# Kernel tuning notes

Measured on AMD Instinct MI355X. Metric: run time of the kernel, lower is better.

The kernel has to match this reference:

```python
import jax, jax.numpy as jnp
import numpy as np

N, E = 50000, 500000
HID, H, D = 128, 8, 16
ED, EGD = 32, 64


def _ln(x, g, b):
    m = x.mean(-1, keepdims=True)
    v = ((x - m) ** 2).mean(-1, keepdims=True)
    return (x - m) / jnp.sqrt(v + 1e-5) * g + b


def _gelu(x):
    return jax.nn.gelu(x, approximate=False)  # torch nn.GELU default (erf)


def setup_inputs() -> dict:
    key = jax.random.key(0)
    ks = jax.random.split(key, 24)
    s = lambda k, shape, scale=0.05: jax.random.normal(k, shape, jnp.float32) * scale
    inp = {
        "x": jax.random.normal(ks[0], (N, HID), jnp.float32),
        "edge_attr": jax.random.normal(ks[1], (E, ED), jnp.float32),
        "gamma": jax.random.uniform(ks[2], (N, HID), jnp.float32),
        "beta": jax.random.normal(ks[3], (N, HID), jnp.float32) * 0.1,
        "Wq": s(ks[4], (HID, H * D)),
        "Wk": s(ks[5], (HID, H * D)),
        "Wv": s(ks[6], (HID, H * D)),
        "Wo": s(ks[7], (H * D, HID)),
        "bo": jnp.zeros((HID,), jnp.float32),
        "ea_w1": s(ks[8], (ED, EGD)), "ea_b1": jnp.zeros((EGD,), jnp.float32),
        "ea_w2": s(ks[9], (EGD, H)), "ea_b2": jnp.zeros((H,), jnp.float32),
        "eg_w1": s(ks[10], (ED, EGD)), "eg_b1": jnp.zeros((EGD,), jnp.float32),
        "eg_w2": s(ks[11], (EGD, H * D)), "eg_b2": jnp.zeros((H * D,), jnp.float32),
        "ln1_g": jnp.ones((HID,), jnp.float32), "ln1_b": jnp.zeros((HID,), jnp.float32),
        "ln2_g": jnp.ones((HID,), jnp.float32), "ln2_b": jnp.zeros((HID,), jnp.float32),
        "ffn_w1": s(ks[12], (HID, 2 * HID)), "ffn_b1": jnp.zeros((2 * HID,), jnp.float32),
        "ffn_w2": s(ks[13], (2 * HID, HID)), "ffn_b2": jnp.zeros((HID,), jnp.float32),
        "edge_index": jax.random.randint(ks[14], (2, E), 0, N, jnp.int32),
    }
    return inp


def reference(x, edge_attr, gamma, beta, Wq, Wk, Wv, Wo, bo,
              ea_w1, ea_b1, ea_w2, ea_b2, eg_w1, eg_b1, eg_w2, eg_b2,
              ln1_g, ln1_b, ln2_g, ln2_b, ffn_w1, ffn_b1, ffn_w2, ffn_b2,
              edge_index):
    n = x.shape[0]
    src, dst = edge_index[0], edge_index[1]
    xn = _ln(x, ln1_g, ln1_b)
    Q = (xn @ Wq).reshape(n, H, D)
    K = (xn @ Wk).reshape(n, H, D)
    V = (xn @ Wv).reshape(n, H, D)
    # per-edge attention logits [E, H]
    logits = (Q[dst] * K[src]).sum(-1) * (D ** -0.5)
    logits = logits + (_gelu(edge_attr @ ea_w1 + ea_b1) @ ea_w2 + ea_b2)
    # sparse softmax over edges sharing a destination; torch version
    # initializes max buffer to zeros (include_self), so clamp max at 0
    m = jnp.maximum(jax.ops.segment_max(logits, dst, num_segments=n), 0.0)
    ex = jnp.exp(logits - m[dst])
    ssum = jax.ops.segment_sum(ex, dst, num_segments=n)
    attn = ex / (ssum[dst] + 1e-10)
    gate = jax.nn.sigmoid(_gelu(edge_attr @ eg_w1 + eg_b1) @ eg_w2 + eg_b2).reshape(-1, H, D)
    weighted = attn[..., None] * (gate * V[src])  # [E, H, D]
    agg = jax.ops.segment_sum(weighted, dst, num_segments=n).reshape(n, H * D)
    out = agg @ Wo + bo
    out = gamma * out + beta
    x = x + out
    x2 = _ln(x, ln2_g, ln2_b)
    f = _gelu(x2 @ ffn_w1 + ffn_b1) @ ffn_w2 + ffn_b2
    return x + f
```

## Files before the change

kernel.cpp:

```cpp
#include <hip/hip_runtime.h>

constexpr int N   = 50000;
constexpr int E   = 500000;
constexpr int HID = 128;
constexpr int NH  = 8;
constexpr int ED  = 32;
constexpr int EGD = 64;
constexpr int NB  = (N + 255) / 256;

typedef short  bf16x8 __attribute__((ext_vector_type(8)));
typedef float  f32x4  __attribute__((ext_vector_type(4)));

__device__ __forceinline__ float gelu_f(float v) {
    float u = v * v;
    float a = v * fmaf(u, -0.07135481283f, -1.5957691216f);
    float e = __expf(a);
    return v * __builtin_amdgcn_rcpf(1.f + e);
}
__device__ __forceinline__ float sigm_f(float v) {
    float e = __expf(-v);
    return __builtin_amdgcn_rcpf(1.f + e);
}
__device__ __forceinline__ unsigned short f2bf(float f) {
    unsigned int u = __float_as_uint(f);
    return (unsigned short)((u + 0x7fffu + ((u >> 16) & 1u)) >> 16);
}
__device__ __forceinline__ unsigned int cvt_pk_bf16(float lo, float hi) {
    unsigned int r;
    asm("v_cvt_pk_bf16_f32 %0, %1, %2" : "=v"(r) : "v"(lo), "v"(hi));
    return r;
}
__device__ __forceinline__ float dot2(unsigned int a, unsigned int b) {
    float al = __uint_as_float(a << 16), ah = __uint_as_float(a & 0xffff0000u);
    float bl = __uint_as_float(b << 16), bh = __uint_as_float(b & 0xffff0000u);
    return al * bl + ah * bh;
}

__global__ __launch_bounds__(256) void k_cvt(
    const float* __restrict__ Wq, const float* __restrict__ Wk,
    const float* __restrict__ Wv, const float* __restrict__ Wo,
    const float* __restrict__ fw1, const float* __restrict__ fw2,
    const float* __restrict__ ea_w1, const float* __restrict__ ea_w2,
    const float* __restrict__ eg_w1, const float* __restrict__ eg_w2,
    unsigned short* __restrict__ dst)
{
    int f = blockIdx.x * 256 + threadIdx.x;
    if (f >= 18048) return;
    const float* W; int KT, srcN, base;
    if      (f < 2048)  { W = Wq;    KT = 4; srcN = 128; base = 0; }
    else if (f < 4096)  { W = Wk;    KT = 4; srcN = 128; base = 2048; }
    else if (f < 6144)  { W = Wv;    KT = 4; srcN = 128; base = 4096; }
    else if (f < 8192)  { W = Wo;    KT = 4; srcN = 128; base = 6144; }
    else if (f < 12288) { W = fw1;   KT = 4; srcN = 256; base = 8192; }
    else if (f < 16384) { W = fw2;   KT = 8; srcN = 128; base = 12288; }
    else if (f < 16640) { W = ea_w1; KT = 1; srcN = 64;  base = 16384; }
    else if (f < 16768) { W = ea_w2; KT = 2; srcN = 8;   base = 16640; }
    else if (f < 17024) { W = eg_w1; KT = 1; srcN = 64;  base = 16768; }
    else                { W = eg_w2; KT = 2; srcN = 128; base = 17024; }
    int fl = f - base, lane = fl & 63, t = fl >> 6;
    int ks = t % KT, nt = t / KT;
    int n  = nt * 16 + (lane & 15);
    int k0 = ks * 32 + (lane >> 4) * 8;
    union { unsigned short u[8]; uint4 v; } o;
#pragma unroll
    for (int j = 0; j < 8; j++)
        o.u[j] = (n < srcN) ? f2bf(W[(size_t)(k0 + j) * srcN + n]) : (unsigned short)0;
    *(uint4*)(dst + (size_t)f * 8) = o.v;
}

__global__ __launch_bounds__(256) void k_ln_qkv_mfma(
    const float* __restrict__ x, const float* __restrict__ g1, const float* __restrict__ b1,
    const unsigned short* __restrict__ wqkv,
    unsigned short* __restrict__ Q, unsigned short* __restrict__ K, unsigned short* __restrict__ V)
{
    __shared__ unsigned short xn_lds[64 * 128];
    const int tid = threadIdx.x;
    const int nodeBase = blockIdx.x * 64;

    {
        int nl = tid >> 2, q = tid & 3;
        int gn = nodeBase + nl; if (gn >= N) gn = N - 1;
        const float4* xp = (const float4*)(x + (size_t)gn * HID + q * 32);
        float xv[32]; float s = 0.f, ss = 0.f;
#pragma unroll
        for (int i = 0; i < 8; i++) {
            float4 t = xp[i];
            xv[4*i] = t.x; xv[4*i+1] = t.y; xv[4*i+2] = t.z; xv[4*i+3] = t.w;
        }
#pragma unroll
        for (int i = 0; i < 32; i++) { s += xv[i]; ss += xv[i] * xv[i]; }
        s += __shfl_xor(s, 1); ss += __shfl_xor(ss, 1);
        s += __shfl_xor(s, 2); ss += __shfl_xor(ss, 2);
        float mean = s * (1.f / HID);
        float ri = rsqrtf(ss * (1.f / HID) - mean * mean + 1e-5f);
#pragma unroll
        for (int j = 0; j < 4; j++) {
            union { unsigned short u[8]; uint4 v4; } o;
#pragma unroll
            for (int c = 0; c < 8; c++) {
                int col = q * 32 + j * 8 + c;
                o.u[c] = f2bf((xv[j*8+c] - mean) * ri * g1[col] + b1[col]);
            }
            int phys = (q * 4 + j) ^ (nl & 15);
            *(uint4*)&xn_lds[nl * 128 + phys * 8] = o.v4;
        }
    }
    __syncthreads();

    const int lane = tid & 63, w = tid >> 6, lm = lane & 15, kb = lane >> 4;
    bf16x8 af[4];
#pragma unroll
    for (int ks = 0; ks < 4; ks++)
        af[ks] = *(const bf16x8*)&xn_lds[(w * 16 + lm) * 128 + ((ks * 4 + kb) ^ lm) * 8];

    for (int nt = 0; nt < 24; nt++) {
        f32x4 c = {0.f, 0.f, 0.f, 0.f};
#pragma unroll
        for (int ks = 0; ks < 4; ks++)
            c = __builtin_amdgcn_mfma_f32_16x16x32_bf16(
                    af[ks], *(const bf16x8*)&wqkv[((size_t)(nt * 4 + ks) * 64 + lane) * 8],
                    c, 0, 0, 0);
        unsigned short* O = (nt < 8) ? Q : ((nt < 16) ? K : V);
        int cc = (nt & 7) * 16 + lm;
#pragma unroll
        for (int r = 0; r < 4; r++) {
            int node = nodeBase + w * 16 + kb * 4 + r;
            if (node < N) O[(size_t)node * HID + cc] = f2bf(c[r]);
        }
    }
}

__global__ __launch_bounds__(256) void k_hist(const int* __restrict__ ei, int* __restrict__ cnt) {
    int e = blockIdx.x * 256 + threadIdx.x;
    if (e < E) atomicAdd(&cnt[ei[E + e]], 1);
}

__global__ __launch_bounds__(256) void k_bsum(const int* __restrict__ cnt, int* __restrict__ bsum) {
    int i = blockIdx.x * 256 + threadIdx.x;
    int v = (i < N) ? cnt[i] : 0;
#pragma unroll
    for (int m = 1; m < 64; m <<= 1) v += __shfl_xor(v, m);
    __shared__ int ws4[4];
    if ((threadIdx.x & 63) == 0) ws4[threadIdx.x >> 6] = v;
    __syncthreads();
    if (threadIdx.x == 0) bsum[blockIdx.x] = ws4[0] + ws4[1] + ws4[2] + ws4[3];
}

__global__ __launch_bounds__(256) void k_scan_b(const int* __restrict__ bsum, int* __restrict__ boff) {
    __shared__ int s[256];
    int t = threadIdx.x;
    int v = (t < NB) ? bsum[t] : 0;
    s[t] = v; __syncthreads();
    for (int off = 1; off < 256; off <<= 1) {
        int add = (t >= off) ? s[t - off] : 0;
        __syncthreads();
        s[t] += add;
        __syncthreads();
    }
    if (t < NB) boff[t] = s[t] - v;
}

__global__ __launch_bounds__(256) void k_scan_final(
    const int* __restrict__ cnt, const int* __restrict__ boff,
    int* __restrict__ starts, int* __restrict__ cursor)
{
    __shared__ int s[256];
    int t = threadIdx.x, i = blockIdx.x * 256 + t;
    int v = (i < N) ? cnt[i] : 0;
    s[t] = v; __syncthreads();
    for (int off = 1; off < 256; off <<= 1) {
        int add = (t >= off) ? s[t - off] : 0;
        __syncthreads();
        s[t] += add;
        __syncthreads();
    }
    int ex = boff[blockIdx.x] + s[t] - v;
    if (i < N) {
        starts[i] = ex;
        cursor[i] = ex;
        if (i == N - 1) starts[N] = ex + v;
    }
}

__global__ __launch_bounds__(256) void k_scatter(
    const int* __restrict__ ei, int* __restrict__ cursor, uint4* __restrict__ esd)
{
    int e = blockIdx.x * 256 + threadIdx.x;
    if (e < E) {
        int src = ei[e], dst = ei[E + e];
        int p = atomicAdd(&cursor[dst], 1);
        esd[p] = make_uint4((unsigned)src, (unsigned)dst, (unsigned)e, 0u);
    }
}

__global__ __launch_bounds__(256) void k_edge(
    const float* __restrict__ edge_attr, const uint4* __restrict__ esd,
    const unsigned short* __restrict__ Qb, const unsigned short* __restrict__ Kb,
    const unsigned short* __restrict__ Vb,
    const unsigned short* __restrict__ w1ea, const float* __restrict__ b1ea,
    const unsigned short* __restrict__ w2ea, const float* __restrict__ b2ea,
    const unsigned short* __restrict__ w1eg, const float* __restrict__ b1eg,
    const unsigned short* __restrict__ w2eg, const float* __restrict__ b2eg,
    float* __restrict__ logit_s, unsigned int* __restrict__ gv)
{
    __shared__ unsigned short ea_lds[256 * 32];
    __shared__ unsigned short sc_lds[4 * 16 * 64];
    __shared__ int perm_lds[256];
    __shared__ int src_lds[256];
    float* st16 = (float*)ea_lds;

    const int tid   = threadIdx.x;
    const int jBase = blockIdx.x * 256;
    const int lane  = tid & 63;
    const int wv    = tid >> 6;
    const int wBase = wv * 64;
    const int lm    = lane & 15;
    const int kb    = lane >> 4;
    const int rowq  = kb * 4;

    const int j  = jBase + tid;
    const int jj = (j < E) ? j : E - 1;
    const uint4 r4 = esd[jj];
    {
        perm_lds[tid] = (int)r4.z;
        src_lds[tid]  = (int)r4.x;
    }
    __syncthreads();

#pragma unroll
    for (int it = 0; it < 8; it++) {
        int idx = it * 256 + tid;
        int el = idx >> 3, c = (idx & 7) * 4;
        int ge = perm_lds[el];
        float4 v = *(const float4*)(edge_attr + (size_t)ge * ED + c);
        int g = ((c >> 3) ^ (el & 3));
        *(uint2*)&ea_lds[el * 32 + g * 8 + (c & 7)] =
            make_uint2(cvt_pk_bf16(v.x, v.y), cvt_pk_bf16(v.z, v.w));
    }
    __syncthreads();

    unsigned short* sc = &sc_lds[wv * 1024];

#pragma unroll 1
    for (int et = 0; et < 4; et++) {
        const int am = wBase + et * 16 + lm;
        const bf16x8 a1 = *(const bf16x8*)&ea_lds[am * 32 + (kb ^ (am & 3)) * 8];

        {
            f32x4 acc[4];
#pragma unroll
            for (int nt = 0; nt < 4; nt++) {
                f32x4 z = {0.f, 0.f, 0.f, 0.f};
                acc[nt] = __builtin_amdgcn_mfma_f32_16x16x32_bf16(
                    a1, *(const bf16x8*)&w1ea[(nt * 64 + lane) * 8], z, 0, 0, 0);
            }
#pragma unroll
            for (int nt = 0; nt < 4; nt++) {
                float bias = b1ea[nt * 16 + lm];
#pragma unroll
                for (int r = 0; r < 4; r++) {
                    int el = rowq + r;
                    int kg = nt * 2 + (lm >> 3);
                    sc[el * 64 + ((kg ^ (el & 7)) * 8) + (lm & 7)] =
                        f2bf(gelu_f(acc[nt][r] + bias));
                }
            }
        }
        {
            bf16x8 f0 = *(const bf16x8*)&sc[lm * 64 + ((kb ^ (lm & 7)) * 8)];
            bf16x8 f1 = *(const bf16x8*)&sc[lm * 64 + (((4 + kb) ^ (lm & 7)) * 8)];
            float bias = b2ea[lm & 7];
            f32x4 acc = {bias, bias, bias, bias};
            acc = __builtin_amdgcn_mfma_f32_16x16x32_bf16(
                f0, *(const bf16x8*)&w2ea[(0 * 64 + lane) * 8], acc, 0, 0, 0);
            acc = __builtin_amdgcn_mfma_f32_16x16x32_bf16(
                f1, *(const bf16x8*)&w2ea[(1 * 64 + lane) * 8], acc, 0, 0, 0);
            if (lm < 8) {
#pragma unroll
                for (int r = 0; r < 4; r++)
                    st16[(wBase + et * 16 + rowq + r) * 16 + lm] = acc[r];
            }
        }
        {
            f32x4 acc[4];
#pragma unroll
            for (int nt = 0; nt < 4; nt++) {
                f32x4 z = {0.f, 0.f, 0.f, 0.f};
                acc[nt] = __builtin_amdgcn_mfma_f32_16x16x32_bf16(
                    a1, *(const bf16x8*)&w1eg[(nt * 64 + lane) * 8], z, 0, 0, 0);
            }
#pragma unroll
            for (int nt = 0; nt < 4; nt++) {
                float bias = b1eg[nt * 16 + lm];
#pragma unroll
                for (int r = 0; r < 4; r++) {
                    int el = rowq + r;
                    int kg = nt * 2 + (lm >> 3);
                    sc[el * 64 + ((kg ^ (el & 7)) * 8) + (lm & 7)] =
                        f2bf(gelu_f(acc[nt][r] + bias));
                }
            }
        }
        {
            bf16x8 h0 = *(const bf16x8*)&sc[lm * 64 + ((kb ^ (lm & 7)) * 8)];
            bf16x8 h1 = *(const bf16x8*)&sc[lm * 64 + (((4 + kb) ^ (lm & 7)) * 8)];
            const int e   = jBase + wBase + et * 16 + lm;
            const int src = src_lds[wBase + et * 16 + lm];
            const unsigned short* vrow = Vb + (size_t)src * HID;
            const bool ok = (e < E);
            unsigned int* gvo = gv + (size_t)e * 64 + kb * 2;
#pragma unroll
            for (int mt = 0; mt < 8; mt++) {
                float4 b4 = *(const float4*)&b2eg[mt * 16 + rowq];
                f32x4 acc = {b4.x, b4.y, b4.z, b4.w};
                acc = __builtin_amdgcn_mfma_f32_16x16x32_bf16(
                    *(const bf16x8*)&w2eg[((mt * 2 + 0) * 64 + lane) * 8], h0, acc, 0, 0, 0);
                acc = __builtin_amdgcn_mfma_f32_16x16x32_bf16(
                    *(const bf16x8*)&w2eg[((mt * 2 + 1) * 64 + lane) * 8], h1, acc, 0, 0, 0);
                uint2 vv = *(const uint2*)(vrow + mt * 16 + rowq);
                float w0 = sigm_f(acc[0]) * __uint_as_float(vv.x << 16);
                float w1 = sigm_f(acc[1]) * __uint_as_float(vv.x & 0xffff0000u);
                float w2 = sigm_f(acc[2]) * __uint_as_float(vv.y << 16);
                float w3 = sigm_f(acc[3]) * __uint_as_float(vv.y & 0xffff0000u);
                uint2 o = make_uint2(cvt_pk_bf16(w0, w1), cvt_pk_bf16(w2, w3));
                if (ok) *(uint2*)(gvo + mt * 8) = o;
            }
        }
    }

    {
        if (j < E) {
            int src = (int)r4.x, dst = (int)r4.y;
            const uint4* qp = (const uint4*)(Qb + (size_t)dst * HID);
            const uint4* kp = (const uint4*)(Kb + (size_t)src * HID);
            float lg[8];
#pragma unroll
            for (int h = 0; h < 8; h++) {
                float dot = 0.f;
#pragma unroll
                for (int t = 0; t < 2; t++) {
                    uint4 q = qp[h * 2 + t], k4 = kp[h * 2 + t];
                    dot += dot2(q.x, k4.x) + dot2(q.y, k4.y) + dot2(q.z, k4.z) + dot2(q.w, k4.w);
                }
                lg[h] = __expf(fminf(st16[tid * 16 + h] + 0.25f * dot, 80.f));
            }
            float4* op = (float4*)(logit_s + (size_t)j * NH);
            op[0] = make_float4(lg[0], lg[1], lg[2], lg[3]);
            op[1] = make_float4(lg[4], lg[5], lg[6], lg[7]);
        }
    }
}

__global__ __launch_bounds__(256) void k_agg2(
    const int* __restrict__ starts, const unsigned int* __restrict__ gv,
    const float* __restrict__ logit_s, float* __restrict__ agg)
{
    int wave = threadIdx.x >> 6, lane = threadIdx.x & 63;
    int dst = blockIdx.x * 4 + wave;
    if (dst >= N) return;
    int s0 = starts[dst], s1 = starts[dst + 1];
    int head = lane >> 3;
    float ssum = 0.f, ax = 0.f, ay = 0.f;
#pragma unroll 4
    for (int j = s0; j < s1; j++) {
        float e = logit_s[(size_t)j * NH + head];
        unsigned int u = gv[(size_t)j * 64 + lane];
        ssum += e;
        ax += e * __uint_as_float(u << 16);
        ay += e * __uint_as_float(u & 0xffff0000u);
    }
    float rs = __builtin_amdgcn_rcpf(ssum + 1e-10f);
    float2* o = (float2*)(agg + (size_t)dst * HID + lane * 2);
    *o = make_float2(ax * rs, ay * rs);
}

__global__ __launch_bounds__(256) void k_node_out_mfma(
    const float* __restrict__ x, const float* __restrict__ gamma, const float* __restrict__ beta,
    const unsigned short* __restrict__ wo_f, const float* __restrict__ bo,
    const float* __restrict__ g2, const float* __restrict__ b2,
    const unsigned short* __restrict__ fw1_f, const float* __restrict__ fb1,
    const unsigned short* __restrict__ fw2_f, const float* __restrict__ fb2,
    const float* __restrict__ agg, float* __restrict__ out)
{
    __shared__ unsigned short a_lds[64 * 128];
    __shared__ unsigned short f1_lds[64 * 256];
    const int tid = threadIdx.x;
    const int nodeBase = blockIdx.x * 64;

    {
        int nl = tid >> 2, q = tid & 3;
        int gn = nodeBase + nl; if (gn >= N) gn = N - 1;
        const float4* ap = (const float4*)(agg + (size_t)gn * HID + q * 32);
#pragma unroll
        for (int j = 0; j < 4; j++) {
            float4 t0 = ap[2 * j], t1 = ap[2 * j + 1];
            uint4 o;
            o.x = cvt_pk_bf16(t0.x, t0.y); o.y = cvt_pk_bf16(t0.z, t0.w);
            o.z = cvt_pk_bf16(t1.x, t1.y); o.w = cvt_pk_bf16(t1.z, t1.w);
            int phys = (q * 4 + j) ^ (nl & 15);
            *(uint4*)&a_lds[nl * 128 + phys * 8] = o;
        }
    }
    __syncthreads();

    const int lane = tid & 63, w = tid >> 6, lm = lane & 15, kb = lane >> 4;
    const int rowLoc = w * 16;

    f32x4 xo[8];
    {
        bf16x8 af[4];
#pragma unroll
        for (int ks = 0; ks < 4; ks++)
            af[ks] = *(const bf16x8*)&a_lds[(rowLoc + lm) * 128 + ((ks * 4 + kb) ^ lm) * 8];
#pragma unroll
        for (int nt = 0; nt < 8; nt++) {
            f32x4 c = {0.f, 0.f, 0.f, 0.f};
#pragma unroll
            for (int ks = 0; ks < 4; ks++)
                c = __builtin_amdgcn_mfma_f32_16x16x32_bf16(
                        af[ks], *(const bf16x8*)&wo_f[((size_t)(nt * 4 + ks) * 64 + lane) * 8],
                        c, 0, 0, 0);
            xo[nt] = c;
        }
    }

    float x1v[8][4];
#pragma unroll
    for (int nt = 0; nt < 8; nt++) {
        int col = nt * 16 + lm;
        float boc = bo[col];
#pragma unroll
        for (int r = 0; r < 4; r++) {
            int node = nodeBase + rowLoc + kb * 4 + r; if (node >= N) node = N - 1;
            size_t idx = (size_t)node * HID + col;
            x1v[nt][r] = x[idx] + gamma[idx] * (xo[nt][r] + boc) + beta[idx];
        }
    }

    float s4[4] = {0,0,0,0}, q4[4] = {0,0,0,0};
#pragma unroll
    for (int nt = 0; nt < 8; nt++)
#pragma unroll
        for (int r = 0; r < 4; r++) { s4[r] += x1v[nt][r]; q4[r] += x1v[nt][r] * x1v[nt][r]; }
#pragma unroll
    for (int m = 1; m < 16; m <<= 1)
#pragma unroll
        for (int r = 0; r < 4; r++) { s4[r] += __shfl_xor(s4[r], m); q4[r] += __shfl_xor(q4[r], m); }
    float mu4[4], ri4[4];
#pragma unroll
    for (int r = 0; r < 4; r++) {
        float mu = s4[r] * (1.f / HID);
        mu4[r] = mu;
        ri4[r] = rsqrtf(q4[r] * (1.f / HID) - mu * mu + 1e-5f);
    }

#pragma unroll
    for (int nt = 0; nt < 8; nt++) {
        int col = nt * 16 + lm;
        float g2c = g2[col], b2c = b2[col];
#pragma unroll
        for (int r = 0; r < 4; r++) {
            float xn = (x1v[nt][r] - mu4[r]) * ri4[r] * g2c + b2c;
            int row = rowLoc + kb * 4 + r;
            int g = col >> 3;
            a_lds[row * 128 + (g ^ (row & 15)) * 8 + (col & 7)] = f2bf(xn);
        }
    }
    __syncthreads();

    {
        bf16x8 af[4];
#pragma unroll
        for (int ks = 0; ks < 4; ks++)
            af[ks] = *(const bf16x8*)&a_lds[(rowLoc + lm) * 128 + ((ks * 4 + kb) ^ lm) * 8];
#pragma unroll
        for (int nt = 0; nt < 16; nt++) {
            f32x4 c = {0.f, 0.f, 0.f, 0.f};
#pragma unroll
            for (int ks = 0; ks < 4; ks++)
                c = __builtin_amdgcn_mfma_f32_16x16x32_bf16(
                        af[ks], *(const bf16x8*)&fw1_f[((size_t)(nt * 4 + ks) * 64 + lane) * 8],
                        c, 0, 0, 0);
            int col = nt * 16 + lm;
            float fbc = fb1[col];
#pragma unroll
            for (int r = 0; r < 4; r++) {
                int row = rowLoc + kb * 4 + r;
                int g = col >> 3;
                int phys = (g & 16) | ((g ^ (row & 15)) & 15);
                f1_lds[row * 256 + phys * 8 + (col & 7)] = f2bf(gelu_f(c[r] + fbc));
            }
        }
    }
    __syncthreads();

    {
        bf16x8 af[8];
#pragma unroll
        for (int ks = 0; ks < 8; ks++) {
            int g = ks * 4 + kb;
            int phys = (g & 16) | ((g ^ lm) & 15);
            af[ks] = *(const bf16x8*)&f1_lds[(rowLoc + lm) * 256 + phys * 8];
        }
#pragma unroll
        for (int nt = 0; nt < 8; nt++) {
            f32x4 c = {0.f, 0.f, 0.f, 0.f};
#pragma unroll
            for (int ks = 0; ks < 8; ks++)
                c = __builtin_amdgcn_mfma_f32_16x16x32_bf16(
                        af[ks], *(const bf16x8*)&fw2_f[((size_t)(nt * 8 + ks) * 64 + lane) * 8],
                        c, 0, 0, 0);
            int col = nt * 16 + lm;
            float fbc = fb2[col];
#pragma unroll
            for (int r = 0; r < 4; r++) {
                int node = nodeBase + rowLoc + kb * 4 + r;
                if (node < N) out[(size_t)node * HID + col] = x1v[nt][r] + c[r] + fbc;
            }
        }
    }
}

extern "C" void kernel_launch(void* const* d_in, const int* in_sizes, int n_in,
                              void* d_out, int out_size, void* d_ws, size_t ws_size,
                              hipStream_t stream)
{
    const float* x         = (const float*)d_in[0];
    const float* edge_attr = (const float*)d_in[1];
    const float* gamma     = (const float*)d_in[2];
    const float* beta      = (const float*)d_in[3];
    const float* Wq        = (const float*)d_in[4];
    const float* Wk        = (const float*)d_in[5];
    const float* Wv        = (const float*)d_in[6];
    const float* Wo        = (const float*)d_in[7];
    const float* bo        = (const float*)d_in[8];
    const float* ea_w1     = (const float*)d_in[9];
    const float* ea_b1     = (const float*)d_in[10];
    const float* ea_w2     = (const float*)d_in[11];
    const float* ea_b2     = (const float*)d_in[12];
    const float* eg_w1     = (const float*)d_in[13];
    const float* eg_b1     = (const float*)d_in[14];
    const float* eg_w2     = (const float*)d_in[15];
    const float* eg_b2     = (const float*)d_in[16];
    const float* ln1_g     = (const float*)d_in[17];
    const float* ln1_b     = (const float*)d_in[18];
    const float* ln2_g     = (const float*)d_in[19];
    const float* ln2_b     = (const float*)d_in[20];
    const float* fw1       = (const float*)d_in[21];
    const float* fb1       = (const float*)d_in[22];
    const float* fw2       = (const float*)d_in[23];
    const float* fb2       = (const float*)d_in[24];
    const int*   ei        = (const int*)d_in[25];

    char* wsb = (char*)d_ws;
    size_t off = 0;
    auto alloc = [&](size_t bytes) { void* p = wsb + off; off += (bytes + 255) & ~(size_t)255; return p; };

    unsigned short* Qb = (unsigned short*)alloc((size_t)N * HID * 2);
    unsigned short* Kb = (unsigned short*)alloc((size_t)N * HID * 2);
    unsigned short* Vb = (unsigned short*)alloc((size_t)N * HID * 2);
    float* logit_s = (float*)alloc((size_t)E * NH * 4);
    float* aggb    = (float*)alloc((size_t)N * HID * 4);
    int*   cnt     = (int*)alloc((size_t)N * 4);
    int*   starts  = (int*)alloc((size_t)(N + 1) * 4);
    int*   cursor  = (int*)alloc((size_t)N * 4);
    int*   bsum    = (int*)alloc((size_t)NB * 4);
    int*   boff    = (int*)alloc((size_t)NB * 4);
    uint4* esd     = (uint4*)alloc((size_t)E * 16);
    unsigned int*   gvb   = (unsigned int*)alloc((size_t)E * 64 * 4);
    unsigned short* fragW = (unsigned short*)alloc((size_t)18048 * 8 * 2);
    float* outp = (float*)d_out;

    unsigned short* wqkv_f = fragW;
    unsigned short* wo_f   = fragW + (size_t)6144  * 8;
    unsigned short* fw1_f  = fragW + (size_t)8192  * 8;
    unsigned short* fw2_f  = fragW + (size_t)12288 * 8;
    unsigned short* w1ea_f = fragW + (size_t)16384 * 8;
    unsigned short* w2ea_f = fragW + (size_t)16640 * 8;
    unsigned short* w1eg_f = fragW + (size_t)16768 * 8;
    unsigned short* w2eg_f = fragW + (size_t)17024 * 8;

    hipMemsetAsync(cnt, 0, (size_t)N * sizeof(int), stream);

    const int EB = (E + 255) / 256;
    const int NBLK = (N + 63) / 64;
    k_cvt<<<(18048 + 255) / 256, 256, 0, stream>>>(Wq, Wk, Wv, Wo, fw1, fw2,
                                                   ea_w1, ea_w2, eg_w1, eg_w2, fragW);
    k_ln_qkv_mfma<<<NBLK, 256, 0, stream>>>(x, ln1_g, ln1_b, wqkv_f, Qb, Kb, Vb);
    k_hist<<<EB, 256, 0, stream>>>(ei, cnt);
    k_bsum<<<NB, 256, 0, stream>>>(cnt, bsum);
    k_scan_b<<<1, 256, 0, stream>>>(bsum, boff);
    k_scan_final<<<NB, 256, 0, stream>>>(cnt, boff, starts, cursor);
    k_scatter<<<EB, 256, 0, stream>>>(ei, cursor, esd);
    k_edge<<<EB, 256, 0, stream>>>(edge_attr, esd, Qb, Kb, Vb,
                                   w1ea_f, ea_b1, w2ea_f, ea_b2,
                                   w1eg_f, eg_b1, w2eg_f, eg_b2,
                                   logit_s, gvb);
    k_agg2<<<(N + 3) / 4, 256, 0, stream>>>(starts, gvb, logit_s, aggb);
    k_node_out_mfma<<<NBLK, 256, 0, stream>>>(x, gamma, beta, wo_f, bo, ln2_g, ln2_b,
                                              fw1_f, fb1, fw2_f, fb2, aggb, outp);
}
```

Baseline: 544.9 us.

## Use single-wave blocks for node MFMA kernels and add k_edge occupancy hint

The LayerNorm+QKV and node-output/FFN kernels now run as 64-thread, 16-node blocks instead of 256-thread, 64-node blocks. Each block is a single wavefront, so the __syncthreads barriers between the LDS staging and MFMA phases are dropped and LDS use per block shrinks, allowing more blocks per CU. k_edge gets a min-blocks-per-CU launch bound of 4, which pushes the compiler to limit registers for more occupancy, and a block-offset parameter, currently 0. Risks are register spills in k_edge and reliance on intra-wave LDS ordering without an explicit barrier.

After: 572.2 us. 5.0% more time.

```diff
diff --git a/kernel.cpp b/kernel.cpp
--- a/kernel.cpp
+++ b/kernel.cpp
@@ -68,14 +68,14 @@
     *(uint4*)(dst + (size_t)f * 8) = o.v;
 }
 
-__global__ __launch_bounds__(256) void k_ln_qkv_mfma(
+__global__ __launch_bounds__(64) void k_ln_qkv_mfma(
     const float* __restrict__ x, const float* __restrict__ g1, const float* __restrict__ b1,
     const unsigned short* __restrict__ wqkv,
     unsigned short* __restrict__ Q, unsigned short* __restrict__ K, unsigned short* __restrict__ V)
 {
-    __shared__ unsigned short xn_lds[64 * 128];
+    __shared__ unsigned short xn_lds[16 * 128];
     const int tid = threadIdx.x;
-    const int nodeBase = blockIdx.x * 64;
+    const int nodeBase = blockIdx.x * 16;
 
     {
         int nl = tid >> 2, q = tid & 3;
@@ -105,13 +105,12 @@
             *(uint4*)&xn_lds[nl * 128 + phys * 8] = o.v4;
         }
     }
-    __syncthreads();
-
-    const int lane = tid & 63, w = tid >> 6, lm = lane & 15, kb = lane >> 4;
+
+    const int lane = tid, lm = lane & 15, kb = lane >> 4;
     bf16x8 af[4];
 #pragma unroll
     for (int ks = 0; ks < 4; ks++)
-        af[ks] = *(const bf16x8*)&xn_lds[(w * 16 + lm) * 128 + ((ks * 4 + kb) ^ lm) * 8];
+        af[ks] = *(const bf16x8*)&xn_lds[lm * 128 + ((ks * 4 + kb) ^ lm) * 8];
 
     for (int nt = 0; nt < 24; nt++) {
         f32x4 c = {0.f, 0.f, 0.f, 0.f};
@@ -124,7 +123,7 @@
         int cc = (nt & 7) * 16 + lm;
 #pragma unroll
         for (int r = 0; r < 4; r++) {
-            int node = nodeBase + w * 16 + kb * 4 + r;
+            int node = nodeBase + kb * 4 + r;
             if (node < N) O[(size_t)node * HID + cc] = f2bf(c[r]);
         }
     }
@@ -193,7 +192,8 @@
     }
 }
 
-__global__ __launch_bounds__(256) void k_edge(
+__global__ __launch_bounds__(256, 4) void k_edge(
+    const int bOff,
     const float* __restrict__ edge_attr, const uint4* __restrict__ esd,
     const unsigned short* __restrict__ Qb, const unsigned short* __restrict__ Kb,
     const unsigned short* __restrict__ Vb,
@@ -210,7 +210,7 @@
     float* st16 = (float*)ea_lds;
 
     const int tid   = threadIdx.x;
-    const int jBase = blockIdx.x * 256;
+    const int jBase = (blockIdx.x + bOff) * 256;
     const int lane  = tid & 63;
     const int wv    = tid >> 6;
     const int wBase = wv * 64;
@@ -374,7 +374,7 @@
     *o = make_float2(ax * rs, ay * rs);
 }
 
-__global__ __launch_bounds__(256) void k_node_out_mfma(
+__global__ __launch_bounds__(64) void k_node_out_mfma(
     const float* __restrict__ x, const float* __restrict__ gamma, const float* __restrict__ beta,
     const unsigned short* __restrict__ wo_f, const float* __restrict__ bo,
     const float* __restrict__ g2, const float* __restrict__ b2,
@@ -382,10 +382,10 @@
     const unsigned short* __restrict__ fw2_f, const float* __restrict__ fb2,
     const float* __restrict__ agg, float* __restrict__ out)
 {
-    __shared__ unsigned short a_lds[64 * 128];
-    __shared__ unsigned short f1_lds[64 * 256];
+    __shared__ unsigned short a_lds[16 * 128];
+    __shared__ unsigned short f1_lds[16 * 256];
     const int tid = threadIdx.x;
-    const int nodeBase = blockIdx.x * 64;
+    const int nodeBase = blockIdx.x * 16;
 
     {
         int nl = tid >> 2, q = tid & 3;
@@ -401,17 +401,15 @@
             *(uint4*)&a_lds[nl * 128 + phys * 8] = o;
         }
     }
-    __syncthreads();
-
-    const int lane = tid & 63, w = tid >> 6, lm = lane & 15, kb = lane >> 4;
-    const int rowLoc = w * 16;
+
+    const int lane = tid, lm = lane & 15, kb = lane >> 4;
 
     f32x4 xo[8];
     {
         bf16x8 af[4];
 #pragma unroll
         for (int ks = 0; ks < 4; ks++)
-            af[ks] = *(const bf16x8*)&a_lds[(rowLoc + lm) * 128 + ((ks * 4 + kb) ^ lm) * 8];
+            af[ks] = *(const bf16x8*)&a_lds[lm * 128 + ((ks * 4 + kb) ^ lm) * 8];
 #pragma unroll
         for (int nt = 0; nt < 8; nt++) {
             f32x4 c = {0.f, 0.f, 0.f, 0.f};
@@ -431,7 +429,7 @@
         float boc = bo[col];
 #pragma unroll
         for (int r = 0; r < 4; r++) {
-            int node = nodeBase + rowLoc + kb * 4 + r; if (node >= N) node = N - 1;
+            int node = nodeBase + kb * 4 + r; if (node >= N) node = N - 1;
             size_t idx = (size_t)node * HID + col;
             x1v[nt][r] = x[idx] + gamma[idx] * (xo[nt][r] + boc) + beta[idx];
         }
@@ -461,18 +459,17 @@
 #pragma unroll
         for (int r = 0; r < 4; r++) {
             float xn = (x1v[nt][r] - mu4[r]) * ri4[r] * g2c + b2c;
-            int row = rowLoc + kb * 4 + r;
+            int row = kb * 4 + r;
             int g = col >> 3;
             a_lds[row * 128 + (g ^ (row & 15)) * 8 + (col & 7)] = f2bf(xn);
         }
     }
-    __syncthreads();
 
     {
         bf16x8 af[4];
 #pragma unroll
         for (int ks = 0; ks < 4; ks++)
-            af[ks] = *(const bf16x8*)&a_lds[(rowLoc + lm) * 128 + ((ks * 4 + kb) ^ lm) * 8];
+            af[ks] = *(const bf16x8*)&a_lds[lm * 128 + ((ks * 4 + kb) ^ lm) * 8];
 #pragma unroll
         for (int nt = 0; nt < 16; nt++) {
             f32x4 c = {0.f, 0.f, 0.f, 0.f};
@@ -485,14 +482,13 @@
             float fbc = fb1[col];
 #pragma unroll
             for (int r = 0; r < 4; r++) {
-                int row = rowLoc + kb * 4 + r;
+                int row = kb * 4 + r;
                 int g = col >> 3;
                 int phys = (g & 16) | ((g ^ (row & 15)) & 15);
                 f1_lds[row * 256 + phys * 8 + (col & 7)] = f2bf(gelu_f(c[r] + fbc));
             }
         }
     }
-    __syncthreads();
 
     {
         bf16x8 af[8];
@@ -500,7 +496,7 @@
         for (int ks = 0; ks < 8; ks++) {
             int g = ks * 4 + kb;
             int phys = (g & 16) | ((g ^ lm) & 15);
-            af[ks] = *(const bf16x8*)&f1_lds[(rowLoc + lm) * 256 + phys * 8];
+            af[ks] = *(const bf16x8*)&f1_lds[lm * 256 + phys * 8];
         }
 #pragma unroll
         for (int nt = 0; nt < 8; nt++) {
@@ -514,7 +510,7 @@
             float fbc = fb2[col];
 #pragma unroll
             for (int r = 0; r < 4; r++) {
-                int node = nodeBase + rowLoc + kb * 4 + r;
+                int node = nodeBase + kb * 4 + r;
                 if (node < N) out[(size_t)node * HID + col] = x1v[nt][r] + c[r] + fbc;
             }
         }
@@ -583,20 +579,20 @@
     hipMemsetAsync(cnt, 0, (size_t)N * sizeof(int), stream);
 
     const int EB = (E + 255) / 256;
-    const int NBLK = (N + 63) / 64;
+    const int NBLK16 = (N + 15) / 16;
     k_cvt<<<(18048 + 255) / 256, 256, 0, stream>>>(Wq, Wk, Wv, Wo, fw1, fw2,
                                                    ea_w1, ea_w2, eg_w1, eg_w2, fragW);
-    k_ln_qkv_mfma<<<NBLK, 256, 0, stream>>>(x, ln1_g, ln1_b, wqkv_f, Qb, Kb, Vb);
+    k_ln_qkv_mfma<<<NBLK16, 64, 0, stream>>>(x, ln1_g, ln1_b, wqkv_f, Qb, Kb, Vb);
     k_hist<<<EB, 256, 0, stream>>>(ei, cnt);
     k_bsum<<<NB, 256, 0, stream>>>(cnt, bsum);
     k_scan_b<<<1, 256, 0, stream>>>(bsum, boff);
     k_scan_final<<<NB, 256, 0, stream>>>(cnt, boff, starts, cursor);
     k_scatter<<<EB, 256, 0, stream>>>(ei, cursor, esd);
-    k_edge<<<EB, 256, 0, stream>>>(edge_attr, esd, Qb, Kb, Vb,
+    k_edge<<<EB, 256, 0, stream>>>(0, edge_attr, esd, Qb, Kb, Vb,
                                    w1ea_f, ea_b1, w2ea_f, ea_b2,
                                    w1eg_f, eg_b1, w2eg_f, eg_b2,
                                    logit_s, gvb);
     k_agg2<<<(N + 3) / 4, 256, 0, stream>>>(starts, gvb, logit_s, aggb);
-    k_node_out_mfma<<<NBLK, 256, 0, stream>>>(x, gamma, beta, wo_f, bo, ln2_g, ln2_b,
-                                              fw1_f, fb1, fw2_f, fb2, aggb, outp);
-}
+    k_node_out_mfma<<<NBLK16, 64, 0, stream>>>(x, gamma, beta, wo_f, bo, ln2_g, ln2_b,
+                                               fw1_f, fb1, fw2_f, fb2, aggb, outp);
+}
```
